# Optimization experiments

Measured on AMD Instinct MI355X. Metric: run time of the kernel, lower is better.

The kernel has to match this reference:

```python
import jax, jax.numpy as jnp
import numpy as np


def setup_inputs() -> dict:
    key = jax.random.key(0)
    T, B, I, M = 256, 64, 512, 512
    ks = jax.random.split(key, 16)
    kai_i = np.sqrt(2.0 / I)   # kaiming_normal_ fan_in
    kai_m = np.sqrt(2.0 / M)
    return {
        "inputs":   jax.random.normal(ks[0], (T, B, I), jnp.float32),
        "sememe_c": jax.random.normal(ks[1], (T, B, M), jnp.float32),
        "sememe_h": jax.random.normal(ks[2], (T, B, M), jnp.float32),
        "c0":       jax.random.normal(ks[3], (B, M), jnp.float32),
        "h0":       jax.random.normal(ks[4], (B, M), jnp.float32),
        "W_ioux": jax.random.normal(ks[5], (3 * M, I), jnp.float32) * kai_i,
        "b_ioux": jnp.zeros((3 * M,), jnp.float32),
        "W_iouh": jax.random.normal(ks[6], (3 * M, M), jnp.float32) * kai_m,
        "b_iouh": jnp.zeros((3 * M,), jnp.float32),
        "W_ious": jax.random.normal(ks[7], (3 * M, M), jnp.float32) * kai_m,
        "b_ious": jnp.zeros((3 * M,), jnp.float32),
        "W_fx":  jax.random.normal(ks[8],  (M, I), jnp.float32) * kai_i,
        "b_fx":  jnp.zeros((M,), jnp.float32),
        "W_fxs": jax.random.normal(ks[9],  (M, I), jnp.float32) * kai_i,
        "b_fxs": jnp.zeros((M,), jnp.float32),
        "W_fh":  jax.random.normal(ks[10], (M, M), jnp.float32) * kai_m,
        "b_fh":  jnp.zeros((M,), jnp.float32),
        "W_fs":  jax.random.normal(ks[11], (M, M), jnp.float32) * kai_m,
        "b_fs":  jnp.zeros((M,), jnp.float32),
    }


def reference(inputs, sememe_c, sememe_h, c0, h0,
              W_ioux, b_ioux, W_iouh, b_iouh, W_ious, b_ious,
              W_fx, b_fx, W_fxs, b_fxs, W_fh, b_fh, W_fs, b_fs):
    # Precompute all input-side projections with big GEMMs over [T*B, I].
    iou_x = jnp.einsum('tbi,oi->tbo', inputs, W_ioux) + b_ioux   # [T,B,3M]
    fx_all = jnp.einsum('tbi,oi->tbo', inputs, W_fx) + b_fx       # [T,B,M]
    fxs_all = jnp.einsum('tbi,oi->tbo', inputs, W_fxs) + b_fxs    # [T,B,M]

    def step(carry, xs):
        c, h = carry
        iou_x_t, fx_t, fxs_t, sc_t, sh_t = xs
        iou = iou_x_t + h @ W_iouh.T + b_iouh + sh_t @ W_ious.T + b_ious
        i, o, u = jnp.split(iou, 3, axis=1)
        i = jax.nn.sigmoid(i)
        o = jax.nn.sigmoid(o)
        u = jnp.tanh(u)
        f = jax.nn.sigmoid(h @ W_fh.T + b_fh + fx_t)
        f_s = jax.nn.sigmoid(sh_t @ W_fs.T + b_fs + fxs_t)
        c_new = i * u + f * c + f_s * sc_t
        h_new = o * jnp.tanh(c_new)
        return (c_new, h_new), h_new

    (c_T, h_T), output = jax.lax.scan(
        step, (c0, h0), (iou_x, fx_all, fxs_all, sememe_c, sememe_h))
    return output, c_T, h_T
```

## Files before the change

kernel.cpp:

```cpp
#include <hip/hip_runtime.h>
#include <cstdint>
#include <cstddef>


typedef _Float16 half8 __attribute__((ext_vector_type(8)));
typedef _Float16 half4 __attribute__((ext_vector_type(4)));
typedef float    f32x4 __attribute__((ext_vector_type(4)));
typedef unsigned int uint32x4 __attribute__((ext_vector_type(4)));

#define T_STEPS 256
#define B_DIM   64
#define M_DIM   512
#define KA      1024
#define NA      2560
#define MA      16384
#define NWG_REC 64
#define FLAG_STRIDE 32

__device__ __forceinline__ float sigmoidf_fast(float x) {
    return 1.0f / (1.0f + __expf(-x));
}
__device__ __forceinline__ float tanhf_fast(float x) {
    float e = __expf(2.0f * x);
    return 1.0f - 2.0f / (e + 1.0f);
}


__global__ void conv_xs(const float* __restrict__ inp, const float* __restrict__ sh,
                        _Float16* __restrict__ xs) {
    int idx = blockIdx.x * blockDim.x + threadIdx.x;
    const int total = MA * KA / 8;
    if (idx >= total) return;
    int row = idx >> 7;
    int col = (idx & 127) * 8;
    const float* src = (col < 512) ? (inp + (size_t)row * 512 + col)
                                   : (sh  + (size_t)row * 512 + (col - 512));
    f32x4 a = *(const f32x4*)src;
    f32x4 b = *(const f32x4*)(src + 4);
    half8 o;
    o[0]=(_Float16)a[0]; o[1]=(_Float16)a[1]; o[2]=(_Float16)a[2]; o[3]=(_Float16)a[3];
    o[4]=(_Float16)b[0]; o[5]=(_Float16)b[1]; o[6]=(_Float16)b[2]; o[7]=(_Float16)b[3];
    *(half8*)(xs + (size_t)idx * 8) = o;
}

__global__ void conv_w(const float* __restrict__ W_ioux, const float* __restrict__ W_ious,
                       const float* __restrict__ W_fx,   const float* __restrict__ W_fxs,
                       const float* __restrict__ W_fs,   _Float16* __restrict__ wc) {
    int idx = blockIdx.x * blockDim.x + threadIdx.x;
    const int total = NA * KA / 8;
    if (idx >= total) return;
    int n = idx >> 7;
    int col = (idx & 127) * 8;
    const float* src = nullptr;
    if (col < 512) {
        int k = col;
        src = (n < 1536) ? (W_ioux + (size_t)n * 512 + k)
            : (n < 2048) ? (W_fx   + (size_t)(n - 1536) * 512 + k)
                         : (W_fxs  + (size_t)(n - 2048) * 512 + k);
    } else {
        int k = col - 512;
        if (n < 1536)      src = W_ious + (size_t)n * 512 + k;
        else if (n >= 2048) src = W_fs  + (size_t)(n - 2048) * 512 + k;
    }
    half8 o;
    if (src) {
        f32x4 a = *(const f32x4*)src;
        f32x4 b = *(const f32x4*)(src + 4);
        o[0]=(_Float16)a[0]; o[1]=(_Float16)a[1]; o[2]=(_Float16)a[2]; o[3]=(_Float16)a[3];
        o[4]=(_Float16)b[0]; o[5]=(_Float16)b[1]; o[6]=(_Float16)b[2]; o[7]=(_Float16)b[3];
    } else {
        #pragma unroll
        for (int i = 0; i < 8; ++i) o[i] = (_Float16)0.0f;
    }
    *(half8*)(wc + (size_t)idx * 8) = o;
}

__global__ void conv_wr(const float* __restrict__ W_iouh, const float* __restrict__ W_fh,
                        _Float16* __restrict__ wr) {
    int idx = blockIdx.x * blockDim.x + threadIdx.x;
    const int total = 2048 * 512 / 8;
    if (idx >= total) return;
    int n = idx >> 6;
    int col = (idx & 63) * 8;
    int wgs = n >> 5, loc = n & 31;
    int g = (loc >> 4) * 2 + ((loc >> 3) & 1);
    int m = wgs * 8 + (loc & 7);
    const float* src = (g < 3) ? (W_iouh + ((size_t)(g * 512 + m)) * 512 + col)
                               : (W_fh   + (size_t)m * 512 + col);
    f32x4 a = *(const f32x4*)src;
    f32x4 b = *(const f32x4*)(src + 4);
    half8 o;
    o[0]=(_Float16)a[0]; o[1]=(_Float16)a[1]; o[2]=(_Float16)a[2]; o[3]=(_Float16)a[3];
    o[4]=(_Float16)b[0]; o[5]=(_Float16)b[1]; o[6]=(_Float16)b[2]; o[7]=(_Float16)b[3];
    *(half8*)(wr + (size_t)idx * 8) = o;
}

__global__ void conv_h0(const float* __restrict__ h0, unsigned short* __restrict__ hb) {
    int idx = blockIdx.x * blockDim.x + threadIdx.x;
    const int total = B_DIM * M_DIM / 8;
    if (idx >= total) return;
    f32x4 a = *(const f32x4*)(h0 + (size_t)idx * 8);
    f32x4 b = *(const f32x4*)(h0 + (size_t)idx * 8 + 4);
    unsigned short o[8];
    #pragma unroll
    for (int j = 0; j < 4; ++j) {
        _Float16 ha = (_Float16)a[j], hbv = (_Float16)b[j];
        o[j]     = (unsigned short)(__builtin_bit_cast(unsigned short, ha)  & 0xFFFCu);
        o[j + 4] = (unsigned short)(__builtin_bit_cast(unsigned short, hbv) & 0xFFFCu);
    }
    uint32x4 pk;
    pk[0] = o[0] | ((unsigned)o[1] << 16);
    pk[1] = o[2] | ((unsigned)o[3] << 16);
    pk[2] = o[4] | ((unsigned)o[5] << 16);
    pk[3] = o[6] | ((unsigned)o[7] << 16);
    *(uint32x4*)(hb + (size_t)idx * 8) = pk;
}


__global__ __launch_bounds__(256, 2)
void gemm_pre(const _Float16* __restrict__ A, const _Float16* __restrict__ W,
              const float* __restrict__ b_ioux, const float* __restrict__ b_iouh,
              const float* __restrict__ b_ious, const float* __restrict__ b_fx,
              const float* __restrict__ b_fh,   const float* __restrict__ b_fxs,
              const float* __restrict__ b_fs,   const float* __restrict__ smc,
              _Float16* __restrict__ pre, _Float16* __restrict__ addc) {
    __shared__ _Float16 As[128 * 64];
    __shared__ _Float16 Bs[128 * 64];

    const int nwg = 2560;
    int orig = blockIdx.x;
    int wgid = (orig & 7) * (nwg >> 3) + (orig >> 3);
    const int bx = wgid & 127;
    const int by = wgid >> 7;
    const int m0 = bx * 128, n0 = by * 128;

    const int tid = threadIdx.x;
    const int wv = tid >> 6, lane = tid & 63;
    const int lr = lane & 15, lq = lane >> 4;
    const int wr = wv >> 1, wc = wv & 1;

    f32x4 acc[4][4];
    #pragma unroll
    for (int i = 0; i < 4; ++i)
        #pragma unroll
        for (int j = 0; j < 4; ++j)
            #pragma unroll
            for (int r = 0; r < 4; ++r) acc[i][j][r] = 0.0f;

    for (int kt = 0; kt < KA / 64; ++kt) {
        const int k0 = kt * 64;
        #pragma unroll
        for (int j = 0; j < 4; ++j) {
            int L = j * 4096 + wv * 1024 + lane * 16;
            int row = L >> 7;
            int colb = (L & 127) ^ ((row & 7) << 4);
            const char* ga = (const char*)(A + (size_t)(m0 + row) * KA + k0) + colb;
            __builtin_amdgcn_global_load_lds(
                (const __attribute__((address_space(1))) void*)ga,
                (__attribute__((address_space(3))) void*)((char*)As + j * 4096 + wv * 1024),
                16, 0, 0);
            const char* gb = (const char*)(W + (size_t)(n0 + row) * KA + k0) + colb;
            __builtin_amdgcn_global_load_lds(
                (const __attribute__((address_space(1))) void*)gb,
                (__attribute__((address_space(3))) void*)((char*)Bs + j * 4096 + wv * 1024),
                16, 0, 0);
        }
        __syncthreads();

        half8 af[4][2], bf[4][2];
        #pragma unroll
        for (int f = 0; f < 4; ++f) {
            #pragma unroll
            for (int kk = 0; kk < 2; ++kk) {
                {
                    int row = wr * 64 + f * 16 + lr;
                    int byt = row * 128 + (((kk * 32 + lq * 8) * 2) ^ ((row & 7) << 4));
                    af[f][kk] = *(const half8*)((const char*)As + byt);
                }
                {
                    int row = wc * 64 + f * 16 + lr;
                    int byt = row * 128 + (((kk * 32 + lq * 8) * 2) ^ ((row & 7) << 4));
                    bf[f][kk] = *(const half8*)((const char*)Bs + byt);
                }
            }
        }
        #pragma unroll
        for (int kk = 0; kk < 2; ++kk)
            #pragma unroll
            for (int fi = 0; fi < 4; ++fi)
                #pragma unroll
                for (int fj = 0; fj < 4; ++fj)
                    acc[fi][fj] = __builtin_amdgcn_mfma_f32_16x16x32_f16(
                        af[fi][kk], bf[fj][kk], acc[fi][fj], 0, 0, 0);
        __syncthreads();
    }

    #pragma unroll
    for (int fi = 0; fi < 4; ++fi) {
        int row0 = m0 + wr * 64 + fi * 16 + lq * 4;
        int tt = row0 >> 6;
        int b  = row0 & 63;
        #pragma unroll
        for (int fj = 0; fj < 4; ++fj) {
            int col = n0 + wc * 64 + fj * 16 + lr;
            f32x4 v = acc[fi][fj];
            if (col < 2048) {
                int g, mm; float bias;
                if (col < 1536) { g = col >> 9; mm = col & 511;
                                  bias = b_ioux[col] + b_iouh[col] + b_ious[col]; }
                else            { g = 3; mm = col - 1536; bias = b_fx[mm] + b_fh[mm]; }
                half4 hv;
                #pragma unroll
                for (int r = 0; r < 4; ++r) hv[r] = (_Float16)(v[r] + bias);
                *(half4*)(pre + ((((size_t)tt * 4 + g) * 512 + mm) * 64 + b)) = hv;
            } else {
                int mm = col - 2048;
                float bias = b_fxs[mm] + b_fs[mm];
                half4 hv;
                #pragma unroll
                for (int r = 0; r < 4; ++r) {
                    float s  = sigmoidf_fast(v[r] + bias);
                    float sc = smc[((size_t)(tt * 64 + b + r)) * 512 + mm];
                    hv[r] = (_Float16)(s * sc);
                }
                *(half4*)(addc + (((size_t)tt * 512 + mm) * 64 + b)) = hv;
            }
        }
    }
}


__device__ __forceinline__ bool gather_try(const char* bp, unsigned pat,
                                           half8 (&af)[16]) {
    asm volatile(
        "global_load_dwordx4 %0,  %16, off sc0 sc1\n\t"
        "global_load_dwordx4 %1,  %16, off offset:64 sc0 sc1\n\t"
        "global_load_dwordx4 %2,  %16, off offset:128 sc0 sc1\n\t"
        "global_load_dwordx4 %3,  %16, off offset:192 sc0 sc1\n\t"
        "global_load_dwordx4 %4,  %16, off offset:256 sc0 sc1\n\t"
        "global_load_dwordx4 %5,  %16, off offset:320 sc0 sc1\n\t"
        "global_load_dwordx4 %6,  %16, off offset:384 sc0 sc1\n\t"
        "global_load_dwordx4 %7,  %16, off offset:448 sc0 sc1\n\t"
        "global_load_dwordx4 %8,  %16, off offset:512 sc0 sc1\n\t"
        "global_load_dwordx4 %9,  %16, off offset:576 sc0 sc1\n\t"
        "global_load_dwordx4 %10, %16, off offset:640 sc0 sc1\n\t"
        "global_load_dwordx4 %11, %16, off offset:704 sc0 sc1\n\t"
        "global_load_dwordx4 %12, %16, off offset:768 sc0 sc1\n\t"
        "global_load_dwordx4 %13, %16, off offset:832 sc0 sc1\n\t"
        "global_load_dwordx4 %14, %16, off offset:896 sc0 sc1\n\t"
        "global_load_dwordx4 %15, %16, off offset:960 sc0 sc1\n\t"
        "s_waitcnt vmcnt(0)"
        : "=&v"(af[0]),  "=&v"(af[1]),  "=&v"(af[2]),  "=&v"(af[3]),
          "=&v"(af[4]),  "=&v"(af[5]),  "=&v"(af[6]),  "=&v"(af[7]),
          "=&v"(af[8]),  "=&v"(af[9]),  "=&v"(af[10]), "=&v"(af[11]),
          "=&v"(af[12]), "=&v"(af[13]), "=&v"(af[14]), "=&v"(af[15])
        : "v"(bp)
        : "memory");
    unsigned bad = 0;
    #pragma unroll
    for (int j = 0; j < 16; ++j) {
        uint32x4 dv = __builtin_bit_cast(uint32x4, af[j]);
        #pragma unroll
        for (int d = 0; d < 4; ++d)
            bad |= (dv[d] & 0x00030003u) ^ pat;
    }
    return __all(bad == 0);
}

__global__ __launch_bounds__(256, 1)
void lstm_rec(const _Float16* __restrict__ Wr, const _Float16* __restrict__ pre,
              const _Float16* __restrict__ addc, const float* __restrict__ c0,
              unsigned short* __restrict__ hbuf, float* __restrict__ out,
              int* __restrict__ flags) {
    const int wg = blockIdx.x;
    const int tid = threadIdx.x;
    const int wv = tid >> 6, lane = tid & 63;
    const int lr = lane & 15, lq = lane >> 4;
    const int c8 = (lane >> 3) & 1;
    const int m  = wg * 8 + (lane & 7);
    const int b0 = wv * 16 + lq * 4;

    half8 bfr[2][16];
    #pragma unroll
    for (int nt = 0; nt < 2; ++nt)
        #pragma unroll
        for (int kk = 0; kk < 16; ++kk)
            bfr[nt][kk] = *(const half8*)(Wr + ((size_t)(wg * 32 + nt * 16 + lr)) * 512
                                          + kk * 32 + lq * 8);

    float c[4];
    #pragma unroll
    for (int r = 0; r < 4; ++r) c[r] = c0[(size_t)(b0 + r) * 512 + m];

    half4 pv[2], av;
    #pragma unroll
    for (int nt = 0; nt < 2; ++nt) {
        int g = nt * 2 + c8;
        pv[nt] = *(const half4*)(pre + (((size_t)0 * 4 + g) * 512 + m) * 64 + b0);
    }
    av = *(const half4*)(addc + ((size_t)0 * 512 + m) * 64 + b0);

    const size_t rowoff = ((size_t)(wv * 16 + lr) * 512 + lq * 8) * 2;
    const int* myflag = flags + lane * FLAG_STRIDE;

    for (int t = 0; t < T_STEPS; ++t) {
        const char* bp = (const char*)hbuf + (size_t)(t & 1) * 65536 + rowoff;
        const unsigned pat = (unsigned)(t & 3) * 0x00010001u;

        f32x4 acc[2];
        #pragma unroll
        for (int nt = 0; nt < 2; ++nt)
            #pragma unroll
            for (int r = 0; r < 4; ++r) acc[nt][r] = (float)pv[nt][r];
        half4 avc = av;

        if (t + 1 < T_STEPS) {
            #pragma unroll
            for (int nt = 0; nt < 2; ++nt) {
                int g = nt * 2 + c8;
                pv[nt] = *(const half4*)(pre + (((size_t)(t + 1) * 4 + g) * 512 + m) * 64 + b0);
            }
            av = *(const half4*)(addc + ((size_t)(t + 1) * 512 + m) * 64 + b0);
        }

        half8 af[16];
        if (!gather_try(bp, pat, af)) {
            while (true) {
                int v;
                asm volatile("global_load_dword %0, %1, off sc0 sc1\n\t"
                             "s_waitcnt vmcnt(0)"
                             : "=v"(v) : "v"(myflag) : "memory");
                if (__all(v >= t)) break;
                __builtin_amdgcn_s_sleep(1);
            }
            while (!gather_try(bp, pat, af))
                __builtin_amdgcn_s_sleep(1);
        }

        #pragma unroll
        for (int kk = 0; kk < 16; ++kk) {
            acc[0] = __builtin_amdgcn_mfma_f32_16x16x32_f16(af[kk], bfr[0][kk], acc[0], 0, 0, 0);
            acc[1] = __builtin_amdgcn_mfma_f32_16x16x32_f16(af[kk], bfr[1][kk], acc[1], 0, 0, 0);
        }

        float hnew[4];
        #pragma unroll
        for (int r = 0; r < 4; ++r) {
            float raw0 = acc[0][r];
            float raw1 = acc[1][r];
            float s0 = sigmoidf_fast(raw0);
            float v1 = c8 ? sigmoidf_fast(raw1) : tanhf_fast(raw1);
            float sf = __shfl_xor(v1, 8);
            float cn = s0 * v1 + sf * c[r] + (float)avc[r];
            float tc = tanhf_fast(cn);
            float tcx = __shfl_xor(tc, 8);
            if (!c8) c[r] = cn;
            hnew[r] = s0 * tcx;
        }

        if (t == T_STEPS - 1) {
            if (c8) {
                #pragma unroll
                for (int r = 0; r < 4; ++r)
                    out[((size_t)t * B_DIM + b0 + r) * M_DIM + m] = hnew[r];
            }
            size_t base = (size_t)T_STEPS * B_DIM * M_DIM;
            if (!c8) {
                #pragma unroll
                for (int r = 0; r < 4; ++r)
                    out[base + (size_t)(b0 + r) * M_DIM + m] = c[r];
            } else {
                #pragma unroll
                for (int r = 0; r < 4; ++r)
                    out[base + (size_t)B_DIM * M_DIM + (size_t)(b0 + r) * M_DIM + m] = hnew[r];
            }
        } else {
            unsigned short* hw = hbuf + (size_t)((t + 1) & 1) * 32768;
            const unsigned tag1 = (unsigned)((t + 1) & 3);
            if (c8) {
                #pragma unroll
                for (int r = 0; r < 4; ++r) {
                    _Float16 hv = (_Float16)hnew[r];
                    unsigned u = ((unsigned)__builtin_bit_cast(unsigned short, hv)
                                  & 0xFFFCu) | tag1;
                    asm volatile("global_store_short %0, %1, off sc0 sc1"
                                 :: "v"(hw + (size_t)(b0 + r) * 512 + m), "v"(u)
                                 : "memory");
                }
            }
            asm volatile("s_waitcnt vmcnt(0)" ::: "memory");
            __syncthreads();
            if (tid == 0) {
                unsigned fv = (unsigned)(t + 1);
                asm volatile("global_store_dword %0, %1, off sc0 sc1"
                             :: "v"(flags + wg * FLAG_STRIDE), "v"(fv) : "memory");
            }
            if (c8) {
                #pragma unroll
                for (int r = 0; r < 4; ++r)
                    out[((size_t)t * B_DIM + b0 + r) * M_DIM + m] = hnew[r];
            }
        }
    }
}


extern "C" void kernel_launch(void* const* d_in, const int* in_sizes, int n_in,
                              void* d_out, int out_size, void* d_ws, size_t ws_size,
                              hipStream_t stream) {
    const float* inputs  = (const float*)d_in[0];
    const float* smc     = (const float*)d_in[1];
    const float* smh     = (const float*)d_in[2];
    const float* c0      = (const float*)d_in[3];
    const float* h0      = (const float*)d_in[4];
    const float* W_ioux  = (const float*)d_in[5];
    const float* b_ioux  = (const float*)d_in[6];
    const float* W_iouh  = (const float*)d_in[7];
    const float* b_iouh  = (const float*)d_in[8];
    const float* W_ious  = (const float*)d_in[9];
    const float* b_ious  = (const float*)d_in[10];
    const float* W_fx    = (const float*)d_in[11];
    const float* b_fx    = (const float*)d_in[12];
    const float* W_fxs   = (const float*)d_in[13];
    const float* b_fxs   = (const float*)d_in[14];
    const float* W_fh    = (const float*)d_in[15];
    const float* b_fh    = (const float*)d_in[16];
    const float* W_fs    = (const float*)d_in[17];
    const float* b_fs    = (const float*)d_in[18];

    char* ws = (char*)d_ws;
    size_t off = 0;
    auto alloc = [&](size_t bytes) {
        char* p = ws + off;
        off = (off + bytes + 255) & ~(size_t)255;
        return p;
    };
    _Float16* XS   = (_Float16*)alloc((size_t)MA * KA * 2);
    _Float16* Wc   = (_Float16*)alloc((size_t)NA * KA * 2);
    _Float16* Wr   = (_Float16*)alloc((size_t)2048 * 512 * 2);
    unsigned short* hb = (unsigned short*)alloc((size_t)2 * B_DIM * M_DIM * 2);
    _Float16* pre  = (_Float16*)alloc((size_t)T_STEPS * 4 * 512 * 64 * 2);
    _Float16* addc = (_Float16*)alloc((size_t)T_STEPS * 512 * 64 * 2);
    int* flags     = (int*)alloc(NWG_REC * FLAG_STRIDE * sizeof(int));
    if (off > ws_size) return;

    hipMemsetAsync(flags, 0, NWG_REC * FLAG_STRIDE * sizeof(int), stream);
    conv_xs <<<MA * KA / 8 / 256, 256, 0, stream>>>(inputs, smh, XS);
    conv_w  <<<NA * KA / 8 / 256, 256, 0, stream>>>(W_ioux, W_ious, W_fx, W_fxs, W_fs, Wc);
    conv_wr <<<2048 * 512 / 8 / 256, 256, 0, stream>>>(W_iouh, W_fh, Wr);
    conv_h0 <<<B_DIM * M_DIM / 8 / 256, 256, 0, stream>>>(h0, hb);
    gemm_pre<<<2560, 256, 0, stream>>>(XS, Wc, b_ioux, b_iouh, b_ious, b_fx, b_fh,
                                       b_fxs, b_fs, smc, pre, addc);
    lstm_rec<<<NWG_REC, 256, 0, stream>>>(Wr, pre, addc, c0, hb, (float*)d_out, flags);
}
```

Measured before the change: 1.399 ms.

## Split recurrent step into batch-half phases with K-split waves and LDS reduction

The recurrent LSTM kernel now processes the batch in two independent 32-row halves per timestep. Each half has its own set of readiness flags, so one half's h-exchange wait can overlap with the other half's compute across workgroups. Within a workgroup, the 512-long K dimension is split across wave pairs, with partial MFMA sums combined through shared memory. This halves per-wave register-resident weights and shortens the MFMA chain, at the cost of extra workgroup barriers and LDS traffic each phase. The flag is now published without waiting for the other wave's h stores, so consumers rely on the data tags for correctness.

```diff
diff --git a/kernel.cpp b/kernel.cpp
--- a/kernel.cpp
+++ b/kernel.cpp
@@ -23,6 +23,11 @@
 __device__ __forceinline__ float tanhf_fast(float x) {
     float e = __expf(2.0f * x);
     return 1.0f - 2.0f / (e + 1.0f);
+}
+__device__ __forceinline__ void wg_barrier() {
+    asm volatile("" ::: "memory");
+    __builtin_amdgcn_s_barrier();
+    asm volatile("" ::: "memory");
 }
 
 
@@ -230,118 +235,101 @@
 }
 
 
-__device__ __forceinline__ bool gather_try(const char* bp, unsigned pat,
-                                           half8 (&af)[16]) {
+__device__ __forceinline__ bool gather_try8(const char* bp, unsigned pat,
+                                            half8 (&af)[8]) {
     asm volatile(
-        "global_load_dwordx4 %0,  %16, off sc0 sc1\n\t"
-        "global_load_dwordx4 %1,  %16, off offset:64 sc0 sc1\n\t"
-        "global_load_dwordx4 %2,  %16, off offset:128 sc0 sc1\n\t"
-        "global_load_dwordx4 %3,  %16, off offset:192 sc0 sc1\n\t"
-        "global_load_dwordx4 %4,  %16, off offset:256 sc0 sc1\n\t"
-        "global_load_dwordx4 %5,  %16, off offset:320 sc0 sc1\n\t"
-        "global_load_dwordx4 %6,  %16, off offset:384 sc0 sc1\n\t"
-        "global_load_dwordx4 %7,  %16, off offset:448 sc0 sc1\n\t"
-        "global_load_dwordx4 %8,  %16, off offset:512 sc0 sc1\n\t"
-        "global_load_dwordx4 %9,  %16, off offset:576 sc0 sc1\n\t"
-        "global_load_dwordx4 %10, %16, off offset:640 sc0 sc1\n\t"
-        "global_load_dwordx4 %11, %16, off offset:704 sc0 sc1\n\t"
-        "global_load_dwordx4 %12, %16, off offset:768 sc0 sc1\n\t"
-        "global_load_dwordx4 %13, %16, off offset:832 sc0 sc1\n\t"
-        "global_load_dwordx4 %14, %16, off offset:896 sc0 sc1\n\t"
-        "global_load_dwordx4 %15, %16, off offset:960 sc0 sc1\n\t"
+        "global_load_dwordx4 %0, %8, off sc0 sc1\n\t"
+        "global_load_dwordx4 %1, %8, off offset:64 sc0 sc1\n\t"
+        "global_load_dwordx4 %2, %8, off offset:128 sc0 sc1\n\t"
+        "global_load_dwordx4 %3, %8, off offset:192 sc0 sc1\n\t"
+        "global_load_dwordx4 %4, %8, off offset:256 sc0 sc1\n\t"
+        "global_load_dwordx4 %5, %8, off offset:320 sc0 sc1\n\t"
+        "global_load_dwordx4 %6, %8, off offset:384 sc0 sc1\n\t"
+        "global_load_dwordx4 %7, %8, off offset:448 sc0 sc1\n\t"
         "s_waitcnt vmcnt(0)"
-        : "=&v"(af[0]),  "=&v"(af[1]),  "=&v"(af[2]),  "=&v"(af[3]),
-          "=&v"(af[4]),  "=&v"(af[5]),  "=&v"(af[6]),  "=&v"(af[7]),
-          "=&v"(af[8]),  "=&v"(af[9]),  "=&v"(af[10]), "=&v"(af[11]),
-          "=&v"(af[12]), "=&v"(af[13]), "=&v"(af[14]), "=&v"(af[15])
+        : "=&v"(af[0]), "=&v"(af[1]), "=&v"(af[2]), "=&v"(af[3]),
+          "=&v"(af[4]), "=&v"(af[5]), "=&v"(af[6]), "=&v"(af[7])
         : "v"(bp)
         : "memory");
     unsigned bad = 0;
     #pragma unroll
-    for (int j = 0; j < 16; ++j) {
+    for (int j = 0; j < 8; ++j) {
         uint32x4 dv = __builtin_bit_cast(uint32x4, af[j]);
         #pragma unroll
-        for (int d = 0; d < 4; ++d)
-            bad |= (dv[d] & 0x00030003u) ^ pat;
+        for (int d = 0; d < 4; ++d) bad |= (dv[d] & 0x00030003u) ^ pat;
     }
     return __all(bad == 0);
 }
 
-__global__ __launch_bounds__(256, 1)
-void lstm_rec(const _Float16* __restrict__ Wr, const _Float16* __restrict__ pre,
-              const _Float16* __restrict__ addc, const float* __restrict__ c0,
-              unsigned short* __restrict__ hbuf, float* __restrict__ out,
-              int* __restrict__ flags) {
-    const int wg = blockIdx.x;
-    const int tid = threadIdx.x;
-    const int wv = tid >> 6, lane = tid & 63;
-    const int lr = lane & 15, lq = lane >> 4;
-    const int c8 = (lane >> 3) & 1;
-    const int m  = wg * 8 + (lane & 7);
-    const int b0 = wv * 16 + lq * 4;
-
-    half8 bfr[2][16];
-    #pragma unroll
-    for (int nt = 0; nt < 2; ++nt)
-        #pragma unroll
-        for (int kk = 0; kk < 16; ++kk)
-            bfr[nt][kk] = *(const half8*)(Wr + ((size_t)(wg * 32 + nt * 16 + lr)) * 512
-                                          + kk * 32 + lq * 8);
-
-    float c[4];
-    #pragma unroll
-    for (int r = 0; r < 4; ++r) c[r] = c0[(size_t)(b0 + r) * 512 + m];
+template<int G>
+__device__ __forceinline__ void lstm_phase(
+    int t, int wg, int mi, int ki, int lane, int lq, int lr, int c8, int m,
+    const half8 (&bfr)[2][8], float (&c)[4],
+    const _Float16* __restrict__ pre, const _Float16* __restrict__ addc,
+    unsigned short* __restrict__ hbuf, float* __restrict__ out,
+    int* __restrict__ flags, f32x4 (*red)[64][2]) {
+
+    const int rb = G * 32 + mi * 16;
+    const int b0 = rb + lq * 4;
 
     half4 pv[2], av;
-    #pragma unroll
-    for (int nt = 0; nt < 2; ++nt) {
-        int g = nt * 2 + c8;
-        pv[nt] = *(const half4*)(pre + (((size_t)0 * 4 + g) * 512 + m) * 64 + b0);
-    }
-    av = *(const half4*)(addc + ((size_t)0 * 512 + m) * 64 + b0);
-
-    const size_t rowoff = ((size_t)(wv * 16 + lr) * 512 + lq * 8) * 2;
-    const int* myflag = flags + lane * FLAG_STRIDE;
-
-    for (int t = 0; t < T_STEPS; ++t) {
-        const char* bp = (const char*)hbuf + (size_t)(t & 1) * 65536 + rowoff;
-        const unsigned pat = (unsigned)(t & 3) * 0x00010001u;
-
-        f32x4 acc[2];
+    if (ki == 0) {
+        #pragma unroll
+        for (int nt = 0; nt < 2; ++nt) {
+            int g = nt * 2 + c8;
+            pv[nt] = *(const half4*)(pre + (((size_t)t * 4 + g) * 512 + m) * 64 + b0);
+        }
+        av = *(const half4*)(addc + ((size_t)t * 512 + m) * 64 + b0);
+    }
+
+    const char* bp = (const char*)hbuf + (size_t)(t & 1) * 65536
+                     + ((size_t)(rb + lr) * 512 + ki * 256 + lq * 8) * 2;
+    const unsigned pat = (unsigned)(t & 3) * 0x00010001u;
+    half8 af[8];
+    if (!gather_try8(bp, pat, af)) {
+        const int* fp = flags + ((size_t)G * 64 + lane) * FLAG_STRIDE;
+        while (true) {
+            int v;
+            asm volatile("global_load_dword %0, %1, off sc0 sc1\n\t"
+                         "s_waitcnt vmcnt(0)"
+                         : "=v"(v) : "v"(fp) : "memory");
+            if (__all(v >= t)) break;
+            __builtin_amdgcn_s_sleep(1);
+        }
+        while (!gather_try8(bp, pat, af))
+            __builtin_amdgcn_s_sleep(1);
+    }
+
+    f32x4 acc[2];
+    if (ki == 0) {
         #pragma unroll
         for (int nt = 0; nt < 2; ++nt)
             #pragma unroll
             for (int r = 0; r < 4; ++r) acc[nt][r] = (float)pv[nt][r];
-        half4 avc = av;
-
-        if (t + 1 < T_STEPS) {
+    } else {
+        #pragma unroll
+        for (int nt = 0; nt < 2; ++nt)
             #pragma unroll
-            for (int nt = 0; nt < 2; ++nt) {
-                int g = nt * 2 + c8;
-                pv[nt] = *(const half4*)(pre + (((size_t)(t + 1) * 4 + g) * 512 + m) * 64 + b0);
-            }
-            av = *(const half4*)(addc + ((size_t)(t + 1) * 512 + m) * 64 + b0);
-        }
-
-        half8 af[16];
-        if (!gather_try(bp, pat, af)) {
-            while (true) {
-                int v;
-                asm volatile("global_load_dword %0, %1, off sc0 sc1\n\t"
-                             "s_waitcnt vmcnt(0)"
-                             : "=v"(v) : "v"(myflag) : "memory");
-                if (__all(v >= t)) break;
-                __builtin_amdgcn_s_sleep(1);
-            }
-            while (!gather_try(bp, pat, af))
-                __builtin_amdgcn_s_sleep(1);
-        }
-
-        #pragma unroll
-        for (int kk = 0; kk < 16; ++kk) {
-            acc[0] = __builtin_amdgcn_mfma_f32_16x16x32_f16(af[kk], bfr[0][kk], acc[0], 0, 0, 0);
-            acc[1] = __builtin_amdgcn_mfma_f32_16x16x32_f16(af[kk], bfr[1][kk], acc[1], 0, 0, 0);
-        }
+            for (int r = 0; r < 4; ++r) acc[nt][r] = 0.0f;
+    }
+    #pragma unroll
+    for (int kk = 0; kk < 8; ++kk) {
+        acc[0] = __builtin_amdgcn_mfma_f32_16x16x32_f16(af[kk], bfr[0][kk], acc[0], 0, 0, 0);
+        acc[1] = __builtin_amdgcn_mfma_f32_16x16x32_f16(af[kk], bfr[1][kk], acc[1], 0, 0, 0);
+    }
+
+    wg_barrier();
+    if (ki == 1) {
+        red[mi][lane][0] = acc[0];
+        red[mi][lane][1] = acc[1];
+    }
+    asm volatile("s_waitcnt lgkmcnt(0)" ::: "memory");
+    wg_barrier();
+
+    if (ki == 0) {
+        f32x4 p0 = red[mi][lane][0], p1 = red[mi][lane][1];
+        #pragma unroll
+        for (int r = 0; r < 4; ++r) { acc[0][r] += p0[r]; acc[1][r] += p1[r]; }
 
         float hnew[4];
         #pragma unroll
@@ -351,30 +339,14 @@
             float s0 = sigmoidf_fast(raw0);
             float v1 = c8 ? sigmoidf_fast(raw1) : tanhf_fast(raw1);
             float sf = __shfl_xor(v1, 8);
-            float cn = s0 * v1 + sf * c[r] + (float)avc[r];
+            float cn = s0 * v1 + sf * c[r] + (float)av[r];
             float tc = tanhf_fast(cn);
             float tcx = __shfl_xor(tc, 8);
             if (!c8) c[r] = cn;
             hnew[r] = s0 * tcx;
         }
 
-        if (t == T_STEPS - 1) {
-            if (c8) {
-                #pragma unroll
-                for (int r = 0; r < 4; ++r)
-                    out[((size_t)t * B_DIM + b0 + r) * M_DIM + m] = hnew[r];
-            }
-            size_t base = (size_t)T_STEPS * B_DIM * M_DIM;
-            if (!c8) {
-                #pragma unroll
-                for (int r = 0; r < 4; ++r)
-                    out[base + (size_t)(b0 + r) * M_DIM + m] = c[r];
-            } else {
-                #pragma unroll
-                for (int r = 0; r < 4; ++r)
-                    out[base + (size_t)B_DIM * M_DIM + (size_t)(b0 + r) * M_DIM + m] = hnew[r];
-            }
-        } else {
+        if (t < T_STEPS - 1) {
             unsigned short* hw = hbuf + (size_t)((t + 1) & 1) * 32768;
             const unsigned tag1 = (unsigned)((t + 1) & 3);
             if (c8) {
@@ -388,19 +360,76 @@
                                  : "memory");
                 }
             }
-            asm volatile("s_waitcnt vmcnt(0)" ::: "memory");
-            __syncthreads();
-            if (tid == 0) {
+            if (mi == 0 && lane == 0) {
                 unsigned fv = (unsigned)(t + 1);
                 asm volatile("global_store_dword %0, %1, off sc0 sc1"
-                             :: "v"(flags + wg * FLAG_STRIDE), "v"(fv) : "memory");
+                             :: "v"(flags + ((size_t)G * 64 + wg) * FLAG_STRIDE),
+                                "v"(fv) : "memory");
             }
             if (c8) {
                 #pragma unroll
                 for (int r = 0; r < 4; ++r)
                     out[((size_t)t * B_DIM + b0 + r) * M_DIM + m] = hnew[r];
             }
-        }
+        } else {
+            if (c8) {
+                #pragma unroll
+                for (int r = 0; r < 4; ++r)
+                    out[((size_t)t * B_DIM + b0 + r) * M_DIM + m] = hnew[r];
+            }
+            size_t base = (size_t)T_STEPS * B_DIM * M_DIM;
+            if (!c8) {
+                #pragma unroll
+                for (int r = 0; r < 4; ++r)
+                    out[base + (size_t)(b0 + r) * M_DIM + m] = c[r];
+            } else {
+                #pragma unroll
+                for (int r = 0; r < 4; ++r)
+                    out[base + (size_t)B_DIM * M_DIM + (size_t)(b0 + r) * M_DIM + m] = hnew[r];
+            }
+        }
+    }
+}
+
+__global__ __launch_bounds__(256, 1)
+void lstm_rec(const _Float16* __restrict__ Wr, const _Float16* __restrict__ pre,
+              const _Float16* __restrict__ addc, const float* __restrict__ c0,
+              unsigned short* __restrict__ hbuf, float* __restrict__ out,
+              int* __restrict__ flags) {
+    __shared__ f32x4 red[2][64][2];
+
+    const int wg = blockIdx.x;
+    const int tid = threadIdx.x;
+    const int wv = tid >> 6, lane = tid & 63;
+    const int mi = wv >> 1, ki = wv & 1;
+    const int lr = lane & 15, lq = lane >> 4;
+    const int c8 = (lane >> 3) & 1;
+    const int m  = wg * 8 + (lane & 7);
+
+    half8 bfr[2][8];
+    #pragma unroll
+    for (int nt = 0; nt < 2; ++nt)
+        #pragma unroll
+        for (int kk = 0; kk < 8; ++kk)
+            bfr[nt][kk] = *(const half8*)(Wr + ((size_t)(wg * 32 + nt * 16 + lr)) * 512
+                                          + ki * 256 + kk * 32 + lq * 8);
+
+    float cA[4], cB[4];
+    {
+        int b0A = 0  + mi * 16 + lq * 4;
+        int b0B = 32 + mi * 16 + lq * 4;
+        #pragma unroll
+        for (int r = 0; r < 4; ++r) {
+            cA[r] = c0[(size_t)(b0A + r) * 512 + m];
+            cB[r] = c0[(size_t)(b0B + r) * 512 + m];
+        }
+    }
+
+    for (int t = 0; t < T_STEPS; ++t) {
+        lstm_phase<0>(t, wg, mi, ki, lane, lq, lr, c8, m, bfr, cA,
+                      pre, addc, hbuf, out, flags, red);
+        lstm_phase<1>(t, wg, mi, ki, lane, lq, lr, c8, m, bfr, cB,
+                      pre, addc, hbuf, out, flags, red);
     }
 }
 
@@ -441,10 +470,10 @@
     unsigned short* hb = (unsigned short*)alloc((size_t)2 * B_DIM * M_DIM * 2);
     _Float16* pre  = (_Float16*)alloc((size_t)T_STEPS * 4 * 512 * 64 * 2);
     _Float16* addc = (_Float16*)alloc((size_t)T_STEPS * 512 * 64 * 2);
-    int* flags     = (int*)alloc(NWG_REC * FLAG_STRIDE * sizeof(int));
+    int* flags     = (int*)alloc((size_t)2 * NWG_REC * FLAG_STRIDE * sizeof(int));
     if (off > ws_size) return;
 
-    hipMemsetAsync(flags, 0, NWG_REC * FLAG_STRIDE * sizeof(int), stream);
+    hipMemsetAsync(flags, 0, (size_t)2 * NWG_REC * FLAG_STRIDE * sizeof(int), stream);
     conv_xs <<<MA * KA / 8 / 256, 256, 0, stream>>>(inputs, smh, XS);
     conv_w  <<<NA * KA / 8 / 256, 256, 0, stream>>>(W_ioux, W_ious, W_fx, W_fxs, W_fs, Wc);
     conv_wr <<<2048 * 512 / 8 / 256, 256, 0, stream>>>(W_iouh, W_fh, Wr);
```

Result: slower. 1.522 ms (+8.8%).
